# Kernel tuning notes

Measured on AMD Instinct MI355X. Metric: run time of the kernel, lower is better.

## Reference

```python
import jax, jax.numpy as jnp
import numpy as np

EMB, GRU_H, HID = 256, 256, 256


def _gru_dir(x_sbe, h0, W_ih, W_hh, b_ih, b_hh):
    # x_sbe: (S,B,E); W_ih: (3H,E); W_hh: (3H,H); biases: (3H,)
    # PyTorch gate order: r, z, n
    gx = jnp.einsum('sbe,ge->sbg', x_sbe, W_ih) + b_ih  # (S,B,3H) precomputed input gates
    H = W_hh.shape[1]

    def step(h, gx_t):
        gh = h @ W_hh.T + b_hh
        xr, xz, xn = gx_t[..., :H], gx_t[..., H:2 * H], gx_t[..., 2 * H:]
        hr, hz, hn = gh[..., :H], gh[..., H:2 * H], gh[..., 2 * H:]
        r = jax.nn.sigmoid(xr + hr)
        z = jax.nn.sigmoid(xz + hz)
        n = jnp.tanh(xn + r * hn)
        h_new = (1.0 - z) * n + z * h
        return h_new, h_new

    hT, ys = jax.lax.scan(step, h0, gx)
    return ys, hT  # ys: (S,B,H), hT: (B,H)


def setup_inputs() -> dict:
    key = jax.random.key(0)
    ks = jax.random.split(key, 12)
    B, S = 64, 1024
    s = 1.0 / np.sqrt(GRU_H)
    u = lambda k, shp: jax.random.uniform(k, shp, jnp.float32, -s, s)
    return {
        'X': jax.random.normal(ks[0], (B, S, EMB), jnp.float32),
        'W_ih_f': u(ks[1], (3 * GRU_H, EMB)),
        'W_hh_f': u(ks[2], (3 * GRU_H, GRU_H)),
        'b_ih_f': u(ks[3], (3 * GRU_H,)),
        'b_hh_f': u(ks[4], (3 * GRU_H,)),
        'W_ih_b': u(ks[5], (3 * GRU_H, EMB)),
        'W_hh_b': u(ks[6], (3 * GRU_H, GRU_H)),
        'b_ih_b': u(ks[7], (3 * GRU_H,)),
        'b_hh_b': u(ks[8], (3 * GRU_H,)),
        'W_fc': u(ks[9], (HID, 2 * GRU_H)),
        'b_fc': u(ks[10], (HID,)),
    }


def reference(X, W_ih_f, W_hh_f, b_ih_f, b_hh_f, W_ih_b, W_hh_b, b_ih_b, b_hh_b, W_fc, b_fc):
    x = jnp.transpose(X, (1, 0, 2))  # (S,B,E)
    S, B, _ = x.shape
    h0 = jnp.zeros((B, GRU_H), x.dtype)
    out_f, hT_f = _gru_dir(x, h0, W_ih_f, W_hh_f, b_ih_f, b_hh_f)
    out_b_rev, hT_b = _gru_dir(x[::-1], h0, W_ih_b, W_hh_b, b_ih_b, b_hh_b)
    out_b = out_b_rev[::-1]
    outputs = jnp.concatenate([out_f, out_b], axis=-1)  # (S,B,2H)
    hidden_state = jnp.stack([hT_f, hT_b], axis=0)      # (2,B,H)
    outputs = jax.nn.relu(jnp.einsum('sbk,hk->sbh', outputs, W_fc) + b_fc)
    return outputs, hidden_state
```

## Files before the change

### kernel.cpp

```cpp
#include <hip/hip_runtime.h>
#include <hip/hip_fp16.h>


typedef _Float16 f16x8 __attribute__((ext_vector_type(8)));
typedef _Float16 f16x4 __attribute__((ext_vector_type(4)));
typedef float    f32x4 __attribute__((ext_vector_type(4)));

#define MFMA(a,b,c) __builtin_amdgcn_mfma_f32_16x16x32_f16((a),(b),(c),0,0,0)
#define SWZ(r,c)  ((((r)*512)  + (c)) ^ (((r)&7)<<4))
#define SWZ2(r,c) ((((r)*1024) + (c)) ^ (((r)&7)<<4))

#define NLOG2E (-1.442695041f)
#define P2LOG2E (2.885390082f)

__device__ inline f16x8 pack8(float4 a, float4 b){
  f16x8 h;
  h[0]=(_Float16)a.x; h[1]=(_Float16)a.y; h[2]=(_Float16)a.z; h[3]=(_Float16)a.w;
  h[4]=(_Float16)b.x; h[5]=(_Float16)b.y; h[6]=(_Float16)b.z; h[7]=(_Float16)b.w;
  return h;
}
__device__ inline f16x8 pack8s(float4 a, float4 b, float s){
  f16x8 h;
  h[0]=(_Float16)(a.x*s); h[1]=(_Float16)(a.y*s); h[2]=(_Float16)(a.z*s); h[3]=(_Float16)(a.w*s);
  h[4]=(_Float16)(b.x*s); h[5]=(_Float16)(b.y*s); h[6]=(_Float16)(b.z*s); h[7]=(_Float16)(b.w*s);
  return h;
}

__global__ __launch_bounds__(256) void k_gx(
    const float* __restrict__ X,
    const float* __restrict__ Wf, const float* __restrict__ bihf, const float* __restrict__ bhhf,
    const float* __restrict__ Wb, const float* __restrict__ bihb, const float* __restrict__ bhhb,
    _Float16* __restrict__ gxc, int CT, int sbase)
{
  const int tc = blockIdx.x, dir = blockIdx.y;
  const int p = sbase + tc;
  const int t = dir ? (1023 - p) : p;
  const float* __restrict__ Wp = dir ? Wb : Wf;
  const float* __restrict__ bi = dir ? bihb : bihf;
  const float* __restrict__ bh = dir ? bhhb : bhhf;
  __shared__ _Float16 As[64*256];
  __shared__ _Float16 Bs[64*256];
  const int tid = threadIdx.x;
  #pragma unroll
  for (int i = 0; i < 8; ++i) {
    int c = tid + i*256, r = c >> 5, cc = c & 31;
    const float4* s4 = (const float4*)(X + ((size_t)r*1024 + t)*256 + cc*8);
    *(f16x8*)((char*)As + SWZ(r, cc*16)) = pack8(s4[0], s4[1]);
  }
  const int w = tid >> 6, l = tid & 63, lr = l & 15, g = l >> 4;
  const size_t obase = (((size_t)dir*CT + tc)*4 + w) * (size_t)12288;
  #pragma unroll 1
  for (int nt = 0; nt < 12; ++nt) {
    __syncthreads();
    #pragma unroll
    for (int i = 0; i < 8; ++i) {
      int c = tid + i*256, r = c >> 5, cc = c & 31;
      const float4* s4 = (const float4*)(Wp + (size_t)(nt*64 + r)*256 + cc*8);
      *(f16x8*)((char*)Bs + SWZ(r, cc*16)) = pack8(s4[0], s4[1]);
    }
    __syncthreads();
    f32x4 acc[4];
    #pragma unroll
    for (int ct = 0; ct < 4; ++ct) acc[ct] = (f32x4){0.f,0.f,0.f,0.f};
    #pragma unroll
    for (int kk = 0; kk < 8; ++kk) {
      f16x8 af = *(const f16x8*)((const char*)As + SWZ(w*16 + lr, kk*64 + g*16));
      #pragma unroll
      for (int ct = 0; ct < 4; ++ct) {
        f16x8 bfr = *(const f16x8*)((const char*)Bs + SWZ(ct*16 + lr, kk*64 + g*16));
        acc[ct] = MFMA(af, bfr, acc[ct]);
      }
    }
    #pragma unroll
    for (int ct = 0; ct < 4; ++ct) {
      const int col = nt*64 + ct*16 + lr;
      const int gate = col >> 8;
      const float sc = (gate == 2) ? P2LOG2E : NLOG2E;
      const float bv = bi[col] + (gate < 2 ? bh[col] : 0.f);
      const int j = col & 255;
      const int tid2 = (j>>5)*64 + g*16 + (j&15);
      const int off = ((j>>4)&1)*4;
      f16x4 v;
      #pragma unroll
      for (int q = 0; q < 4; ++q) v[q] = (_Float16)((acc[ct][q] + bv)*sc);
      *(f16x4*)(gxc + obase + (size_t)tid2*24 + gate*8 + off) = v;
    }
  }
}

__global__ __launch_bounds__(512, 2) void k_rec(
    const float* __restrict__ Whh_f, const float* __restrict__ bhh_f,
    const float* __restrict__ Whh_b, const float* __restrict__ bhh_b,
    const _Float16* __restrict__ gxc, float* __restrict__ wsh,
    _Float16* __restrict__ out16, float* __restrict__ hidden,
    int CT, int sbase)
{
  const int dir = blockIdx.x & 1;
  const int bsl = blockIdx.x >> 1;
  const int bbase = bsl * 16;
  const float* __restrict__ Whh = dir ? Whh_b : Whh_f;
  const float* __restrict__ bhh = dir ? bhh_b : bhh_f;
  const int tid = threadIdx.x, w = tid >> 6, l = tid & 63;
  const int lr = l & 15, g = l >> 4;
  const int j0 = w * 32;
  f16x8 wf[6][8];
  #pragma unroll
  for (int ct = 0; ct < 6; ++ct) {
    const int colg = (ct>>1)*256 + j0 + (ct&1)*16 + lr;
    const float scl = (ct < 4) ? NLOG2E : P2LOG2E;
    #pragma unroll
    for (int kk = 0; kk < 8; ++kk) {
      const float4* s4 = (const float4*)(Whh + (size_t)colg*256 + kk*32 + g*8);
      wf[ct][kk] = pack8s(s4[0], s4[1], scl);
    }
  }
  const float bn0 = P2LOG2E * bhh[512 + j0 + lr];
  const float bn1 = P2LOG2E * bhh[512 + j0 + 16 + lr];
  __shared__ _Float16 hs[2][4096];
  char* const afp = (char*)hs + l*16;
  char* const hwp = (char*)hs + w*1024 + (lr>>3)*256 + g*64 + (lr&7)*2;
  float hold[2][4];
  if (sbase == 0) {
    *(int4*)((char*)hs + tid*16) = make_int4(0,0,0,0);
    #pragma unroll
    for (int jt = 0; jt < 2; ++jt)
      #pragma unroll
      for (int q = 0; q < 4; ++q) hold[jt][q] = 0.f;
  } else {
    const int r = tid >> 5, kq = tid & 31;
    const float4* s4 = (const float4*)(wsh + ((size_t)(dir*64 + bbase + r))*256 + kq*8);
    *(f16x8*)((char*)hs + (kq>>2)*1024 + (((kq&3)*16) + r)*16) = pack8(s4[0], s4[1]);
    #pragma unroll
    for (int jt = 0; jt < 2; ++jt)
      #pragma unroll
      for (int q = 0; q < 4; ++q)
        hold[jt][q] = wsh[((size_t)(dir*64 + bbase + g*4 + q))*256 + j0 + jt*16 + lr];
  }
  __syncthreads();

  const int t0 = dir ? (1023 - sbase) : sbase;
  char* optr = (char*)out16 + ((size_t)t0*64 + bbase + g*4)*1024
             + (size_t)(dir*256 + j0 + lr)*2;
  const ptrdiff_t ostep = dir ? -(ptrdiff_t)65536 : (ptrdiff_t)65536;
  const _Float16* gp = gxc + ((size_t)(dir*CT)*4 + bsl)*12288 + (size_t)tid*24;
  const ptrdiff_t gstep = 4*12288;

#define REC_STEP(RB)                                                               \
  {                                                                                \
    const f16x8 gv0 = *(const f16x8*)(gp);                                         \
    const f16x8 gv1 = *(const f16x8*)(gp + 8);                                     \
    const f16x8 gv2 = *(const f16x8*)(gp + 16);                                    \
    gp += gstep;                                                                   \
    {                                                                              \
      f32x4 ar = (f32x4){0.f,0.f,0.f,0.f};                                         \
      f32x4 az = (f32x4){0.f,0.f,0.f,0.f};                                         \
      f32x4 an = (f32x4){bn0,bn0,bn0,bn0};                                         \
      _Pragma("unroll")                                                            \
      for (int kk = 0; kk < 8; ++kk) {                                             \
        const f16x8 af = *(const f16x8*)(afp + (RB)*8192 + kk*1024);               \
        ar = MFMA(af, wf[0][kk], ar);                                              \
        az = MFMA(af, wf[2][kk], az);                                              \
        an = MFMA(af, wf[4][kk], an);                                              \
      }                                                                            \
      _Pragma("unroll")                                                            \
      for (int q = 0; q < 4; ++q) {                                                \
        const float rv = __builtin_amdgcn_rcpf(                                    \
            1.f + __builtin_amdgcn_exp2f((float)gv0[q] + ar[q]));                  \
        const float zv = __builtin_amdgcn_rcpf(                                    \
            1.f + __builtin_amdgcn_exp2f((float)gv1[q] + az[q]));                  \
        const float nv = __builtin_fmaf(-2.f, __builtin_amdgcn_rcpf(               \
            1.f + __builtin_amdgcn_exp2f(                                          \
                __builtin_fmaf(rv, an[q], (float)gv2[q]))), 1.f);                  \
        const float h = __builtin_fmaf(zv, hold[0][q] - nv, nv);                   \
        hold[0][q] = h;                                                            \
        const _Float16 hf = (_Float16)h;                                           \
        *(_Float16*)(hwp + ((RB)^1)*8192 + q*16) = hf;                             \
        *(_Float16*)(optr + q*1024) = hf;                                          \
      }                                                                            \
    }                                                                              \
    {                                                                              \
      f32x4 ar = (f32x4){0.f,0.f,0.f,0.f};                                         \
      f32x4 az = (f32x4){0.f,0.f,0.f,0.f};                                         \
      f32x4 an = (f32x4){bn1,bn1,bn1,bn1};                                         \
      _Pragma("unroll")                                                            \
      for (int kk = 0; kk < 8; ++kk) {                                             \
        const f16x8 af = *(const f16x8*)(afp + (RB)*8192 + kk*1024);               \
        ar = MFMA(af, wf[1][kk], ar);                                              \
        az = MFMA(af, wf[3][kk], az);                                              \
        an = MFMA(af, wf[5][kk], an);                                              \
      }                                                                            \
      _Pragma("unroll")                                                            \
      for (int q = 0; q < 4; ++q) {                                                \
        const float rv = __builtin_amdgcn_rcpf(                                    \
            1.f + __builtin_amdgcn_exp2f((float)gv0[4+q] + ar[q]));                \
        const float zv = __builtin_amdgcn_rcpf(                                    \
            1.f + __builtin_amdgcn_exp2f((float)gv1[4+q] + az[q]));                \
        const float nv = __builtin_fmaf(-2.f, __builtin_amdgcn_rcpf(               \
            1.f + __builtin_amdgcn_exp2f(                                          \
                __builtin_fmaf(rv, an[q], (float)gv2[4+q]))), 1.f);                \
        const float h = __builtin_fmaf(zv, hold[1][q] - nv, nv);                   \
        hold[1][q] = h;                                                            \
        const _Float16 hf = (_Float16)h;                                           \
        *(_Float16*)(hwp + ((RB)^1)*8192 + 512 + q*16) = hf;                       \
        *(_Float16*)(optr + q*1024 + 32) = hf;                                     \
      }                                                                            \
    }                                                                              \
    optr += ostep;                                                                 \
    asm volatile("s_waitcnt lgkmcnt(0)" ::: "memory");                             \
    __builtin_amdgcn_s_barrier();                                                  \
    asm volatile("" ::: "memory");                                                 \
  }

  #pragma unroll 1
  for (int sc = 0; sc < CT; sc += 2) {
    REC_STEP(0)
    REC_STEP(1)
  }
#undef REC_STEP

  if (sbase + CT == 1024) {
    #pragma unroll
    for (int jt = 0; jt < 2; ++jt)
      #pragma unroll
      for (int q = 0; q < 4; ++q)
        hidden[((size_t)(dir*64 + bbase + g*4 + q))*256 + j0 + jt*16 + lr] = hold[jt][q];
  } else {
    #pragma unroll
    for (int jt = 0; jt < 2; ++jt)
      #pragma unroll
      for (int q = 0; q < 4; ++q)
        wsh[((size_t)(dir*64 + bbase + g*4 + q))*256 + j0 + jt*16 + lr] = hold[jt][q];
  }
}

__global__ __launch_bounds__(256) void k_fc(
    const _Float16* __restrict__ h16, const float* __restrict__ Wfc,
    const float* __restrict__ bfc, float* __restrict__ out)
{
  const int mt = blockIdx.x;
  __shared__ _Float16 As[64*512];
  const int tid = threadIdx.x, w = tid >> 6, l = tid & 63;
  const int lr = l & 15, g = l >> 4;
  #pragma unroll
  for (int i = 0; i < 16; ++i) {
    int c = tid + i*256, r = c >> 6, cc = c & 63;
    *(int4*)((char*)As + SWZ2(r, cc*16)) =
        *(const int4*)((const char*)h16 + ((size_t)mt*64 + r)*1024 + cc*16);
  }
  __syncthreads();
  #pragma unroll 1
  for (int nt = 0; nt < 4; ++nt) {
    f32x4 acc[4];
    #pragma unroll
    for (int ct = 0; ct < 4; ++ct) acc[ct] = (f32x4){0.f,0.f,0.f,0.f};
    #pragma unroll 2
    for (int kk = 0; kk < 16; ++kk) {
      f16x8 af = *(const f16x8*)((const char*)As + SWZ2(w*16 + lr, kk*64 + g*16));
      #pragma unroll
      for (int ct = 0; ct < 4; ++ct) {
        const float4* s4 = (const float4*)(Wfc + (size_t)(nt*64 + ct*16 + lr)*512 + kk*32 + g*8);
        acc[ct] = MFMA(af, pack8(s4[0], s4[1]), acc[ct]);
      }
    }
    #pragma unroll
    for (int ct = 0; ct < 4; ++ct) {
      const int col = nt*64 + ct*16 + lr;
      const float bv = bfc[col];
      #pragma unroll
      for (int q = 0; q < 4; ++q) {
        const int row = w*16 + g*4 + q;
        out[((size_t)mt*64 + row)*256 + col] = fmaxf(acc[ct][q] + bv, 0.f);
      }
    }
  }
}

extern "C" void kernel_launch(void* const* d_in, const int* in_sizes, int n_in,
                              void* d_out, int out_size, void* d_ws, size_t ws_size,
                              hipStream_t stream) {
  const float* X      = (const float*)d_in[0];
  const float* W_ih_f = (const float*)d_in[1];
  const float* W_hh_f = (const float*)d_in[2];
  const float* b_ih_f = (const float*)d_in[3];
  const float* b_hh_f = (const float*)d_in[4];
  const float* W_ih_b = (const float*)d_in[5];
  const float* W_hh_b = (const float*)d_in[6];
  const float* b_ih_b = (const float*)d_in[7];
  const float* b_hh_b = (const float*)d_in[8];
  const float* W_fc   = (const float*)d_in[9];
  const float* b_fc   = (const float*)d_in[10];

  int CT = 256;
  while (CT > 8 && ((size_t)CT*196608 + 131072) > ws_size) CT >>= 1;
  _Float16* gxc = (_Float16*)d_ws;
  float*    wsh = (float*)((char*)d_ws + (size_t)CT*196608);

  _Float16* h16   = (_Float16*)d_out;
  float*    out   = (float*)d_out;
  float*    hidden= (float*)d_out + (size_t)1024*64*256;

  const int NC = 1024 / CT;
  for (int c = 0; c < NC; ++c) {
    k_gx<<<dim3(CT, 2), dim3(256), 0, stream>>>(X, W_ih_f, b_ih_f, b_hh_f,
                                                W_ih_b, b_ih_b, b_hh_b, gxc, CT, c*CT);
    k_rec<<<dim3(8), dim3(512), 0, stream>>>(W_hh_f, b_hh_f, W_hh_b, b_hh_b,
                                             gxc, wsh, h16, hidden, CT, c*CT);
  }
  k_fc<<<dim3(1024), dim3(256), 0, stream>>>(h16, W_fc, b_fc, out);
}
```

Baseline: 2.292 ms.

## Overlap next chunk's input-gate GEMM with current recurrence via double-buffered fused launch

Input-gate projection blocks for chunk c+1 now run in the same launch as the recurrence blocks for chunk c, writing into a second gx buffer, so the serial recurrence no longer waits for a separate gx kernel each chunk. The gx body is moved into a 512-thread block where only 4 waves do MFMA work, and the recurrence waves get a raised priority via s_setprio. The cost is that the workspace must hold two gx buffers, so CT may shrink. The gx blocks also compete with the 8 recurrence blocks for CU resources and memory bandwidth.

```diff
diff --git a/kernel.cpp b/kernel.cpp
--- a/kernel.cpp
+++ b/kernel.cpp
@@ -26,75 +26,99 @@
   return h;
 }
 
-__global__ __launch_bounds__(256) void k_gx(
+__device__ __forceinline__ void gx_body(
+    char* smem, const float* __restrict__ X,
+    const float* __restrict__ Wp, const float* __restrict__ bi, const float* __restrict__ bh,
+    _Float16* __restrict__ gxc, int CT, int tc, int dir, int t)
+{
+  _Float16* As = (_Float16*)smem;
+  _Float16* Bs = (_Float16*)(smem + 32768);
+  const int tid = threadIdx.x;
+  #pragma unroll
+  for (int i = 0; i < 4; ++i) {
+    int c = tid + i*512, r = c >> 5, cc = c & 31;
+    const float4* s4 = (const float4*)(X + ((size_t)r*1024 + t)*256 + cc*8);
+    *(f16x8*)((char*)As + SWZ(r, cc*16)) = pack8(s4[0], s4[1]);
+  }
+  const int w = tid >> 6, l = tid & 63, lr = l & 15, g = l >> 4;
+  const size_t obase = (((size_t)dir*CT + tc)*4 + (w & 3)) * (size_t)12288;
+  #pragma unroll 1
+  for (int nt = 0; nt < 12; ++nt) {
+    __syncthreads();
+    #pragma unroll
+    for (int i = 0; i < 4; ++i) {
+      int c = tid + i*512, r = c >> 5, cc = c & 31;
+      const float4* s4 = (const float4*)(Wp + (size_t)(nt*64 + r)*256 + cc*8);
+      *(f16x8*)((char*)Bs + SWZ(r, cc*16)) = pack8(s4[0], s4[1]);
+    }
+    __syncthreads();
+    if (w < 4) {
+      f32x4 acc[4];
+      #pragma unroll
+      for (int ct = 0; ct < 4; ++ct) acc[ct] = (f32x4){0.f,0.f,0.f,0.f};
+      #pragma unroll
+      for (int kk = 0; kk < 8; ++kk) {
+        f16x8 af = *(const f16x8*)((const char*)As + SWZ(w*16 + lr, kk*64 + g*16));
+        #pragma unroll
+        for (int ct = 0; ct < 4; ++ct) {
+          f16x8 bfr = *(const f16x8*)((const char*)Bs + SWZ(ct*16 + lr, kk*64 + g*16));
+          acc[ct] = MFMA(af, bfr, acc[ct]);
+        }
+      }
+      #pragma unroll
+      for (int ct = 0; ct < 4; ++ct) {
+        const int col = nt*64 + ct*16 + lr;
+        const int gate = col >> 8;
+        const float sc = (gate == 2) ? P2LOG2E : NLOG2E;
+        const float bv = bi[col] + (gate < 2 ? bh[col] : 0.f);
+        const int j = col & 255;
+        const int tid2 = (j>>5)*64 + g*16 + (j&15);
+        const int off = ((j>>4)&1)*4;
+        f16x4 v;
+        #pragma unroll
+        for (int q = 0; q < 4; ++q) v[q] = (_Float16)((acc[ct][q] + bv)*sc);
+        *(f16x4*)(gxc + obase + (size_t)tid2*24 + gate*8 + off) = v;
+      }
+    }
+  }
+}
+
+__global__ __launch_bounds__(512, 2) void k_gx0(
     const float* __restrict__ X,
     const float* __restrict__ Wf, const float* __restrict__ bihf, const float* __restrict__ bhhf,
     const float* __restrict__ Wb, const float* __restrict__ bihb, const float* __restrict__ bhhb,
     _Float16* __restrict__ gxc, int CT, int sbase)
 {
+  __shared__ char smem[65536];
   const int tc = blockIdx.x, dir = blockIdx.y;
   const int p = sbase + tc;
   const int t = dir ? (1023 - p) : p;
-  const float* __restrict__ Wp = dir ? Wb : Wf;
-  const float* __restrict__ bi = dir ? bihb : bihf;
-  const float* __restrict__ bh = dir ? bhhb : bhhf;
-  __shared__ _Float16 As[64*256];
-  __shared__ _Float16 Bs[64*256];
-  const int tid = threadIdx.x;
-  #pragma unroll
-  for (int i = 0; i < 8; ++i) {
-    int c = tid + i*256, r = c >> 5, cc = c & 31;
-    const float4* s4 = (const float4*)(X + ((size_t)r*1024 + t)*256 + cc*8);
-    *(f16x8*)((char*)As + SWZ(r, cc*16)) = pack8(s4[0], s4[1]);
-  }
-  const int w = tid >> 6, l = tid & 63, lr = l & 15, g = l >> 4;
-  const size_t obase = (((size_t)dir*CT + tc)*4 + w) * (size_t)12288;
-  #pragma unroll 1
-  for (int nt = 0; nt < 12; ++nt) {
-    __syncthreads();
-    #pragma unroll
-    for (int i = 0; i < 8; ++i) {
-      int c = tid + i*256, r = c >> 5, cc = c & 31;
-      const float4* s4 = (const float4*)(Wp + (size_t)(nt*64 + r)*256 + cc*8);
-      *(f16x8*)((char*)Bs + SWZ(r, cc*16)) = pack8(s4[0], s4[1]);
-    }
-    __syncthreads();
-    f32x4 acc[4];
-    #pragma unroll
-    for (int ct = 0; ct < 4; ++ct) acc[ct] = (f32x4){0.f,0.f,0.f,0.f};
-    #pragma unroll
-    for (int kk = 0; kk < 8; ++kk) {
-      f16x8 af = *(const f16x8*)((const char*)As + SWZ(w*16 + lr, kk*64 + g*16));
-      #pragma unroll
-      for (int ct = 0; ct < 4; ++ct) {
-        f16x8 bfr = *(const f16x8*)((const char*)Bs + SWZ(ct*16 + lr, kk*64 + g*16));
-        acc[ct] = MFMA(af, bfr, acc[ct]);
-      }
-    }
-    #pragma unroll
-    for (int ct = 0; ct < 4; ++ct) {
-      const int col = nt*64 + ct*16 + lr;
-      const int gate = col >> 8;
-      const float sc = (gate == 2) ? P2LOG2E : NLOG2E;
-      const float bv = bi[col] + (gate < 2 ? bh[col] : 0.f);
-      const int j = col & 255;
-      const int tid2 = (j>>5)*64 + g*16 + (j&15);
-      const int off = ((j>>4)&1)*4;
-      f16x4 v;
-      #pragma unroll
-      for (int q = 0; q < 4; ++q) v[q] = (_Float16)((acc[ct][q] + bv)*sc);
-      *(f16x4*)(gxc + obase + (size_t)tid2*24 + gate*8 + off) = v;
-    }
-  }
-}
-
-__global__ __launch_bounds__(512, 2) void k_rec(
+  gx_body(smem, X, dir ? Wb : Wf, dir ? bihb : bihf, dir ? bhhb : bhhf,
+          gxc, CT, tc, dir, t);
+}
+
+__global__ __launch_bounds__(512, 2) void k_step(
     const float* __restrict__ Whh_f, const float* __restrict__ bhh_f,
     const float* __restrict__ Whh_b, const float* __restrict__ bhh_b,
-    const _Float16* __restrict__ gxc, float* __restrict__ wsh,
+    const _Float16* __restrict__ gxin, float* __restrict__ wsh,
     _Float16* __restrict__ out16, float* __restrict__ hidden,
-    int CT, int sbase)
+    int CT, int sbase,
+    const float* __restrict__ X,
+    const float* __restrict__ Wf, const float* __restrict__ bihf, const float* __restrict__ bhhf,
+    const float* __restrict__ Wb, const float* __restrict__ bihb, const float* __restrict__ bhhb,
+    _Float16* __restrict__ gxout, int sbase_gx, int gx_valid)
 {
+  __shared__ char smem[65536];
+  if (blockIdx.x >= 8) {
+    if (!gx_valid) return;
+    const int b = blockIdx.x - 8;
+    const int tc = b >> 1, dir = b & 1;
+    const int p = sbase_gx + tc;
+    const int t = dir ? (1023 - p) : p;
+    gx_body(smem, X, dir ? Wb : Wf, dir ? bihb : bihf, dir ? bhhb : bhhf,
+            gxout, CT, tc, dir, t);
+    return;
+  }
   const int dir = blockIdx.x & 1;
   const int bsl = blockIdx.x >> 1;
   const int bbase = bsl * 16;
@@ -116,12 +140,12 @@
   }
   const float bn0 = P2LOG2E * bhh[512 + j0 + lr];
   const float bn1 = P2LOG2E * bhh[512 + j0 + 16 + lr];
-  __shared__ _Float16 hs[2][4096];
-  char* const afp = (char*)hs + l*16;
-  char* const hwp = (char*)hs + w*1024 + (lr>>3)*256 + g*64 + (lr&7)*2;
+  char* const hsb = smem;
+  char* const afp = hsb + l*16;
+  char* const hwp = hsb + w*1024 + (lr>>3)*256 + g*64 + (lr&7)*2;
   float hold[2][4];
   if (sbase == 0) {
-    *(int4*)((char*)hs + tid*16) = make_int4(0,0,0,0);
+    *(int4*)(hsb + tid*16) = make_int4(0,0,0,0);
     #pragma unroll
     for (int jt = 0; jt < 2; ++jt)
       #pragma unroll
@@ -129,7 +153,7 @@
   } else {
     const int r = tid >> 5, kq = tid & 31;
     const float4* s4 = (const float4*)(wsh + ((size_t)(dir*64 + bbase + r))*256 + kq*8);
-    *(f16x8*)((char*)hs + (kq>>2)*1024 + (((kq&3)*16) + r)*16) = pack8(s4[0], s4[1]);
+    *(f16x8*)(hsb + (kq>>2)*1024 + (((kq&3)*16) + r)*16) = pack8(s4[0], s4[1]);
     #pragma unroll
     for (int jt = 0; jt < 2; ++jt)
       #pragma unroll
@@ -137,12 +161,13 @@
         hold[jt][q] = wsh[((size_t)(dir*64 + bbase + g*4 + q))*256 + j0 + jt*16 + lr];
   }
   __syncthreads();
+  if (w & 1) __builtin_amdgcn_s_setprio(1);
 
   const int t0 = dir ? (1023 - sbase) : sbase;
   char* optr = (char*)out16 + ((size_t)t0*64 + bbase + g*4)*1024
              + (size_t)(dir*256 + j0 + lr)*2;
   const ptrdiff_t ostep = dir ? -(ptrdiff_t)65536 : (ptrdiff_t)65536;
-  const _Float16* gp = gxc + ((size_t)(dir*CT)*4 + bsl)*12288 + (size_t)tid*24;
+  const _Float16* gp = gxin + ((size_t)(dir*CT)*4 + bsl)*12288 + (size_t)tid*24;
   const ptrdiff_t gstep = 4*12288;
 
 #define REC_STEP(RB)                                                               \
@@ -291,20 +316,26 @@
   const float* b_fc   = (const float*)d_in[10];
 
   int CT = 256;
-  while (CT > 8 && ((size_t)CT*196608 + 131072) > ws_size) CT >>= 1;
-  _Float16* gxc = (_Float16*)d_ws;
-  float*    wsh = (float*)((char*)d_ws + (size_t)CT*196608);
+  while (CT > 8 && (2*(size_t)CT*196608 + 131072) > ws_size) CT >>= 1;
+  const size_t CTB = (size_t)CT*196608;
+  _Float16* buf0 = (_Float16*)d_ws;
+  _Float16* buf1 = (_Float16*)((char*)d_ws + CTB);
+  float*    wsh  = (float*)((char*)d_ws + 2*CTB);
 
   _Float16* h16   = (_Float16*)d_out;
   float*    out   = (float*)d_out;
   float*    hidden= (float*)d_out + (size_t)1024*64*256;
 
   const int NC = 1024 / CT;
+  k_gx0<<<dim3(CT, 2), dim3(512), 0, stream>>>(X, W_ih_f, b_ih_f, b_hh_f,
+                                               W_ih_b, b_ih_b, b_hh_b, buf0, CT, 0);
   for (int c = 0; c < NC; ++c) {
-    k_gx<<<dim3(CT, 2), dim3(256), 0, stream>>>(X, W_ih_f, b_ih_f, b_hh_f,
-                                                W_ih_b, b_ih_b, b_hh_b, gxc, CT, c*CT);
-    k_rec<<<dim3(8), dim3(512), 0, stream>>>(W_hh_f, b_hh_f, W_hh_b, b_hh_b,
-                                             gxc, wsh, h16, hidden, CT, c*CT);
+    _Float16* bin  = (c & 1) ? buf1 : buf0;
+    _Float16* bout = (c & 1) ? buf0 : buf1;
+    k_step<<<dim3(8 + 2*CT), dim3(512), 0, stream>>>(
+        W_hh_f, b_hh_f, W_hh_b, b_hh_b, bin, wsh, h16, hidden, CT, c*CT,
+        X, W_ih_f, b_ih_f, b_hh_f, W_ih_b, b_ih_b, b_hh_b,
+        bout, (c+1)*CT, (c < NC-1) ? 1 : 0);
   }
   k_fc<<<dim3(1024), dim3(256), 0, stream>>>(h16, W_fc, b_fc, out);
 }
```

After: 2.105 ms. 8.2% less time.
